# Performance work log

Measured on AMD Instinct MI355X. Metric: run time of the kernel, lower is better.

## Reference

```python
import jax, jax.numpy as jnp
import numpy as np

NEG_BIG = -9e15

def setup_inputs() -> dict:
    key = jax.random.key(0)
    k1, k2, k3, k4 = jax.random.split(key, 4)
    N, F_in, F_out = 8192, 512, 128
    return {
        "input": jax.random.normal(k1, (N, F_in), dtype=jnp.float32),
        "adj": jax.random.randint(k2, (N, N), 0, 2, dtype=jnp.int32),
        "W": jax.random.normal(k3, (F_in, F_out), dtype=jnp.float32) * 0.05,
        "a": jax.random.normal(k4, (2 * F_out, 1), dtype=jnp.float32) * 0.05,
    }

def reference(input, adj, W, a):
    alpha = 0.2  # LeakyReLU negative slope
    h = input @ W                      # [N, F_out]
    F_out = h.shape[1]
    # concat score decomposition: a^T [h_i || h_j] = h_i @ a1 + h_j @ a2
    a1 = a[:F_out, 0]                  # [F_out]
    a2 = a[F_out:, 0]                  # [F_out]
    e = jax.nn.leaky_relu(h @ a1[:, None] + (h @ a2)[None, :], negative_slope=alpha)  # [N, N]
    e = jnp.where(adj > 0, e, NEG_BIG)
    attention = jax.nn.softmax(e, axis=1)
    h_prime = attention @ h            # [N, F_out]
    return jax.nn.elu(h_prime)         # concat=True
```

## Files before the change

kernel.cpp:

```cpp
#include <hip/hip_runtime.h>
#include <hip/hip_bf16.h>


typedef __attribute__((ext_vector_type(4))) float f32x4;
typedef __attribute__((ext_vector_type(8))) short s16x8;

#define N_NODES 8192
#define F_IN 512
#define F_OUT 128
#define JS 16
#define WCOLS (N_NODES / JS)

static __device__ __forceinline__ short f2bf(float f) {
  __hip_bfloat16 h = __float2bfloat16(f);
  return __builtin_bit_cast(short, h);
}

__global__ __launch_bounds__(256) void kA(const float* __restrict__ W,
    const float* __restrict__ a, unsigned short* __restrict__ WT,
    float* __restrict__ wa) {
  int b = blockIdx.x;
  if (b < 256) {
    int idx = b * 256 + threadIdx.x;
    int k = idx >> 7, f = idx & 127;
    WT[(size_t)f * F_IN + k] = (unsigned short)f2bf(W[idx]);
  } else {
    int k = (b - 256) * 256 + threadIdx.x;
    if (k < F_IN) {
      const float* Wr = W + (size_t)k * F_OUT;
      float d1 = 0.f, d2 = 0.f;
#pragma unroll 8
      for (int f = 0; f < F_OUT; f += 4) {
        f32x4 w  = *(const f32x4*)(Wr + f);
        f32x4 a1 = *(const f32x4*)(a + f);
        f32x4 a2 = *(const f32x4*)(a + F_OUT + f);
        d1 += w[0] * a1[0] + w[1] * a1[1] + w[2] * a1[2] + w[3] * a1[3];
        d2 += w[0] * a2[0] + w[1] * a2[1] + w[2] * a2[2] + w[3] * a2[3];
      }
      wa[k] = d1;
      wa[F_IN + k] = d2;
    }
  }
}

__global__ __launch_bounds__(256) void kB(const int* __restrict__ adj,
    unsigned long long* __restrict__ mask, const float* __restrict__ X,
    const float* __restrict__ wa, const unsigned short* __restrict__ WT,
    f32x4* __restrict__ rowdat, unsigned* __restrict__ pE,
    unsigned short* __restrict__ hT) {
  int b = blockIdx.x;
  int wave = threadIdx.x >> 6, lane = threadIdx.x & 63;

  if (b < 4096) {
    const int nwaves = 4096 * 4;
    int wid = b * 4 + wave;
    const int ntasks = N_NODES * (N_NODES / 256);
    for (int task = wid; task < ntasks; task += nwaves) {
      int row = task >> 5;
      int cg = task & 31;
      const int* p = adj + (size_t)row * N_NODES + cg * 256 + lane;
      int v0 = p[0], v1 = p[64], v2 = p[128], v3 = p[192];
      unsigned long long b0 = __ballot(v0 != 0);
      unsigned long long b1 = __ballot(v1 != 0);
      unsigned long long b2 = __ballot(v2 != 0);
      unsigned long long b3 = __ballot(v3 != 0);
      if (lane == 0) {
        unsigned long long* q = mask + (size_t)row * (N_NODES / 64) + cg * 4;
        ulonglong2 w0; w0.x = b0; w0.y = b1;
        ulonglong2 w1; w1.x = b2; w1.y = b3;
        *(ulonglong2*)(q) = w0;
        *(ulonglong2*)(q + 2) = w1;
      }
    }
  } else if (b < 6144) {
    int i = (b - 4096) * 4 + wave;
    const float* Xr = X + (size_t)i * F_IN + lane * 8;
    f32x4 x0 = ((const f32x4*)Xr)[0];
    f32x4 x1 = ((const f32x4*)Xr)[1];
    f32x4 w10 = ((const f32x4*)(wa + lane * 8))[0];
    f32x4 w11 = ((const f32x4*)(wa + lane * 8))[1];
    f32x4 w20 = ((const f32x4*)(wa + F_IN + lane * 8))[0];
    f32x4 w21 = ((const f32x4*)(wa + F_IN + lane * 8))[1];
    float d1 = 0.f, d2 = 0.f;
#pragma unroll
    for (int e = 0; e < 4; e++) {
      d1 += x0[e] * w10[e] + x1[e] * w11[e];
      d2 += x0[e] * w20[e] + x1[e] * w21[e];
    }
#pragma unroll
    for (int m = 1; m < 64; m <<= 1) {
      d1 += __shfl_xor(d1, m, 64);
      d2 += __shfl_xor(d2, m, 64);
    }
    if (lane == 0) {
      float s1 = d1, s2 = d2;
      f32x4 rd;
      rd[0] = expf(s1);
      rd[1] = expf(0.2f * s1);
      rd[2] = expf(-s1);
      rd[3] = 0.f;
      rowdat[i] = rd;
      unsigned e2  = (unsigned)(unsigned short)f2bf(expf(s2));
      unsigned e2s = (unsigned)(unsigned short)f2bf(expf(0.2f * s2));
      pE[i] = (e2s << 16) | e2;
    }
  } else {
    int lrow = lane & 15, grp = lane >> 4;
    int tile = (b - 6144) * 4 + wave;
    int fb = tile & 7;
    int nb = tile >> 3;
    const unsigned short* Ar = WT + (size_t)(fb * 16 + lrow) * F_IN + grp * 8;
    const float* Br = X + (size_t)(nb * 16 + lrow) * F_IN + grp * 8;

    f32x4 acc = (f32x4)(0.0f);
#pragma unroll
    for (int k0 = 0; k0 < F_IN; k0 += 32) {
      s16x8 af = *(const s16x8*)(Ar + k0);
      f32x4 b0 = *(const f32x4*)(Br + k0);
      f32x4 b1 = *(const f32x4*)(Br + k0 + 4);
      s16x8 bf;
#pragma unroll
      for (int e = 0; e < 4; e++) { bf[e] = f2bf(b0[e]); bf[e + 4] = f2bf(b1[e]); }
      acc = __builtin_amdgcn_mfma_f32_16x16x32_bf16(af, bf, acc, 0, 0, 0);
    }
#pragma unroll
    for (int r = 0; r < 4; r++)
      hT[(size_t)(fb * 16 + grp * 4 + r) * N_NODES + nb * 16 + lrow] =
          (unsigned short)f2bf(acc[r]);
  }
}

__global__ __launch_bounds__(256, 2) void kC(const unsigned* __restrict__ mask32,
    const unsigned short* __restrict__ hT, const f32x4* __restrict__ rowdat,
    const unsigned* __restrict__ pE, float* __restrict__ accws,
    float* __restrict__ denws) {
  __shared__ float red[4][16 * 132];
  __shared__ float sden[4][4][16];

  int wave = threadIdx.x >> 6, lane = threadIdx.x & 63;
  int lrow = lane & 15, grp = lane >> 4;
  int rb = blockIdx.x >> 2;
  int q = blockIdx.x & 3;
  int js = q * 4 + wave;
  int rbase = rb * 64;
  int jlo = js * WCOLS;

  float E1[4], E1s[4], T1[4];
#pragma unroll
  for (int rt = 0; rt < 4; rt++) {
    f32x4 rd = rowdat[rbase + rt * 16 + lrow];
    E1[rt] = rd[0]; E1s[rt] = rd[1]; T1[rt] = rd[2];
  }

  f32x4 acc[4][8];
#pragma unroll
  for (int rt = 0; rt < 4; rt++)
#pragma unroll
    for (int n = 0; n < 8; n++) acc[rt][n] = (f32x4)(0.0f);
  float dsum[4] = {0.f, 0.f, 0.f, 0.f};

#define PROC1(rt, pe, e)                                              \
  {                                                                   \
    unsigned pu = (pe);                                               \
    float E2  = __builtin_bit_cast(float, pu << 16);                  \
    float E2s = __builtin_bit_cast(float, pu & 0xffff0000u);          \
    float sel = (E2 > T1[rt]) ? E1[rt] * E2 : E1s[rt] * E2s;          \
    float p = ((bm >> (e)) & 1u) ? sel : 0.f;                         \
    dsum[rt] += p;                                                    \
    af[rt][e] = f2bf(p);                                              \
  }

  for (int sc = 0; sc < 4; sc++) {
    int jb = jlo + sc * 128;
    uint4 mm[4];
#pragma unroll
    for (int rt = 0; rt < 4; rt++)
      mm[rt] = *(const uint4*)(mask32 +
          (size_t)(rbase + rt * 16 + lrow) * (N_NODES / 32) + jb / 32);

#pragma unroll
    for (int t = 0; t < 4; t++) {
      int jj = jb + t * 32 + grp * 8;
      const uint4* pp = (const uint4*)(pE + jj);
      uint4 P0 = pp[0], P1 = pp[1];
      s16x8 af[4];
#pragma unroll
      for (int rt = 0; rt < 4; rt++) {
        unsigned bm = (mm[rt][t] >> (grp * 8)) & 0xffu;
        PROC1(rt, P0.x, 0); PROC1(rt, P0.y, 1);
        PROC1(rt, P0.z, 2); PROC1(rt, P0.w, 3);
        PROC1(rt, P1.x, 4); PROC1(rt, P1.y, 5);
        PROC1(rt, P1.z, 6); PROC1(rt, P1.w, 7);
      }
#pragma unroll
      for (int n = 0; n < 8; n++) {
        s16x8 bf = *(const s16x8*)(hT + (size_t)(n * 16 + lrow) * N_NODES + jj);
#pragma unroll
        for (int rt = 0; rt < 4; rt++)
          acc[rt][n] =
              __builtin_amdgcn_mfma_f32_16x16x32_bf16(af[rt], bf, acc[rt][n], 0, 0, 0);
      }
    }
  }
#undef PROC1

#pragma unroll
  for (int rt = 0; rt < 4; rt++) {
    float d = dsum[rt];
    d += __shfl_xor(d, 16, 64);
    d += __shfl_xor(d, 32, 64);
    if (lane < 16) sden[wave][rt][lane] = d;
  }

#pragma unroll
  for (int rt = 0; rt < 4; rt++) {
    __syncthreads();
#pragma unroll
    for (int n = 0; n < 8; n++)
#pragma unroll
      for (int r = 0; r < 4; r++)
        red[wave][(grp * 4 + r) * 132 + n * 16 + lrow] = acc[rt][n][r];
    __syncthreads();
    int e0 = threadIdx.x * 8;
    int row16 = e0 >> 7, col = e0 & 127;
    int li = row16 * 132 + col;
    f32x4 s0 = *(f32x4*)&red[0][li] + *(f32x4*)&red[1][li] +
               *(f32x4*)&red[2][li] + *(f32x4*)&red[3][li];
    f32x4 s1 = *(f32x4*)&red[0][li + 4] + *(f32x4*)&red[1][li + 4] +
               *(f32x4*)&red[2][li + 4] + *(f32x4*)&red[3][li + 4];
    float* dst = accws +
        ((size_t)q * N_NODES + rbase + rt * 16 + row16) * F_OUT + col;
    *(f32x4*)dst = s0;
    *(f32x4*)(dst + 4) = s1;
  }
  __syncthreads();
  if (threadIdx.x < 64) {
    int rt = threadIdx.x >> 4, r16 = threadIdx.x & 15;
    float d = sden[0][rt][r16] + sden[1][rt][r16] +
              sden[2][rt][r16] + sden[3][rt][r16];
    denws[q * N_NODES + rbase + threadIdx.x] = d;
  }
}

__global__ void kD(const float* __restrict__ accws,
                   const float* __restrict__ denws, float* __restrict__ out) {
  int idx4 = blockIdx.x * 256 + threadIdx.x;
  int i = idx4 >> 5;
  const int S4 = N_NODES * F_OUT / 4;
  f32x4 s = (f32x4)(0.0f);
  float d = 0.f;
#pragma unroll
  for (int q = 0; q < 4; q++) {
    s += ((const f32x4*)accws)[idx4 + (size_t)q * S4];
    d += denws[i + q * N_NODES];
  }
  f32x4 v = s / d;
#pragma unroll
  for (int e = 0; e < 4; e++) v[e] = v[e] > 0.f ? v[e] : expm1f(v[e]);
  ((f32x4*)out)[idx4] = v;
}

extern "C" void kernel_launch(void* const* d_in, const int* in_sizes, int n_in,
                              void* d_out, int out_size, void* d_ws, size_t ws_size,
                              hipStream_t stream) {
  const float* X   = (const float*)d_in[0];
  const int*   adj = (const int*)d_in[1];
  const float* W   = (const float*)d_in[2];
  const float* a   = (const float*)d_in[3];
  float* out = (float*)d_out;

  char* ws = (char*)d_ws;
  size_t off = 0;
  unsigned short* WT = (unsigned short*)(ws + off); off += (size_t)F_OUT * F_IN * 2;
  unsigned short* hT = (unsigned short*)(ws + off); off += (size_t)F_OUT * N_NODES * 2;
  f32x4* rowdat = (f32x4*)(ws + off); off += (size_t)N_NODES * 16;
  unsigned* pE = (unsigned*)(ws + off); off += (size_t)N_NODES * 4;
  float* wa = (float*)(ws + off); off += (size_t)2 * F_IN * 4;
  unsigned long long* mask = (unsigned long long*)(ws + off);
  off += (size_t)N_NODES * (N_NODES / 64) * 8;
  float* accws = (float*)(ws + off); off += (size_t)4 * N_NODES * F_OUT * 4;
  float* denws = (float*)(ws + off); off += (size_t)4 * N_NODES * 4;
  (void)in_sizes; (void)n_in; (void)out_size; (void)ws_size;

  kA<<<258, 256, 0, stream>>>(W, a, WT, wa);
  kB<<<7168, 256, 0, stream>>>(adj, mask, X, wa, WT, rowdat, pE, hT);
  kC<<<(N_NODES / 64) * 4, 256, 0, stream>>>((const unsigned*)mask, hT,
                                             rowdat, pE, accws, denws);
  kD<<<(N_NODES * F_OUT) / 4 / 256, 256, 0, stream>>>(accws, denws, out);
}
```

Before: 518.7 us.

## Pre-swizzle h into MFMA fragment layout and retile attention kernel

Moves the adjacency bitmask packing into its own kernel and has the staging GEMM write h in a blob layout matching the MFMA B-fragment, so each lane loads its 16 bytes contiguously. The attention kernel is retiled: each wave handles 16 rows by 64 features across half the columns, with 2 column splits instead of 4. This removes the LDS cross-wave reduction and halves the partial-sum workspace. The cost is that the softmax weights (mask, exp, select) are now recomputed by two feature-group waves per row tile, and the mask kernel is serialized ahead of the GEMM.

```diff
diff --git a/kernel.cpp b/kernel.cpp
--- a/kernel.cpp
+++ b/kernel.cpp
@@ -8,12 +8,35 @@
 #define N_NODES 8192
 #define F_IN 512
 #define F_OUT 128
-#define JS 16
-#define WCOLS (N_NODES / JS)
 
 static __device__ __forceinline__ short f2bf(float f) {
   __hip_bfloat16 h = __float2bfloat16(f);
   return __builtin_bit_cast(short, h);
+}
+
+__global__ __launch_bounds__(256) void kMask(const int* __restrict__ adj,
+    unsigned long long* __restrict__ mask) {
+  const int nwaves = gridDim.x * 4;
+  int wid = blockIdx.x * 4 + (threadIdx.x >> 6);
+  int lane = threadIdx.x & 63;
+  const int ntasks = N_NODES * (N_NODES / 256);
+  for (int task = wid; task < ntasks; task += nwaves) {
+    int row = task >> 5;
+    int cg = task & 31;
+    const int* p = adj + (size_t)row * N_NODES + cg * 256 + lane;
+    int v0 = p[0], v1 = p[64], v2 = p[128], v3 = p[192];
+    unsigned long long b0 = __ballot(v0 != 0);
+    unsigned long long b1 = __ballot(v1 != 0);
+    unsigned long long b2 = __ballot(v2 != 0);
+    unsigned long long b3 = __ballot(v3 != 0);
+    if (lane == 0) {
+      unsigned long long* q = mask + (size_t)row * (N_NODES / 64) + cg * 4;
+      ulonglong2 w0; w0.x = b0; w0.y = b1;
+      ulonglong2 w1; w1.x = b2; w1.y = b3;
+      *(ulonglong2*)(q) = w0;
+      *(ulonglong2*)(q + 2) = w1;
+    }
+  }
 }
 
 __global__ __launch_bounds__(256) void kA(const float* __restrict__ W,
@@ -43,37 +66,39 @@
   }
 }
 
-__global__ __launch_bounds__(256) void kB(const int* __restrict__ adj,
-    unsigned long long* __restrict__ mask, const float* __restrict__ X,
+__global__ __launch_bounds__(256) void kStage(const float* __restrict__ X,
     const float* __restrict__ wa, const unsigned short* __restrict__ WT,
     f32x4* __restrict__ rowdat, unsigned* __restrict__ pE,
-    unsigned short* __restrict__ hT) {
+    unsigned short* __restrict__ blob) {
   int b = blockIdx.x;
   int wave = threadIdx.x >> 6, lane = threadIdx.x & 63;
 
-  if (b < 4096) {
-    const int nwaves = 4096 * 4;
-    int wid = b * 4 + wave;
-    const int ntasks = N_NODES * (N_NODES / 256);
-    for (int task = wid; task < ntasks; task += nwaves) {
-      int row = task >> 5;
-      int cg = task & 31;
-      const int* p = adj + (size_t)row * N_NODES + cg * 256 + lane;
-      int v0 = p[0], v1 = p[64], v2 = p[128], v3 = p[192];
-      unsigned long long b0 = __ballot(v0 != 0);
-      unsigned long long b1 = __ballot(v1 != 0);
-      unsigned long long b2 = __ballot(v2 != 0);
-      unsigned long long b3 = __ballot(v3 != 0);
-      if (lane == 0) {
-        unsigned long long* q = mask + (size_t)row * (N_NODES / 64) + cg * 4;
-        ulonglong2 w0; w0.x = b0; w0.y = b1;
-        ulonglong2 w1; w1.x = b2; w1.y = b3;
-        *(ulonglong2*)(q) = w0;
-        *(ulonglong2*)(q + 2) = w1;
-      }
-    }
-  } else if (b < 6144) {
-    int i = (b - 4096) * 4 + wave;
+  if (b < 1024) {
+    int lrow = lane & 15, grp = lane >> 4;
+    int tile = b * 4 + wave;
+    int fb = tile & 7;
+    int nb = tile >> 3;
+    const unsigned short* Ar = WT + (size_t)(fb * 16 + lrow) * F_IN + grp * 8;
+    const float* Br = X + (size_t)(nb * 16 + lrow) * F_IN + grp * 8;
+
+    f32x4 acc = (f32x4)(0.0f);
+#pragma unroll
+    for (int k0 = 0; k0 < F_IN; k0 += 32) {
+      s16x8 af = *(const s16x8*)(Ar + k0);
+      f32x4 b0 = *(const f32x4*)(Br + k0);
+      f32x4 b1 = *(const f32x4*)(Br + k0 + 4);
+      s16x8 bf;
+#pragma unroll
+      for (int e = 0; e < 4; e++) { bf[e] = f2bf(b0[e]); bf[e + 4] = f2bf(b1[e]); }
+      acc = __builtin_amdgcn_mfma_f32_16x16x32_bf16(af, bf, acc, 0, 0, 0);
+    }
+    int cc = (nb & 1) * 16 + lrow;
+    size_t bl = ((size_t)(fb * 256 + (nb >> 1)) * 64 + (cc >> 3) * 16 + grp * 4);
+#pragma unroll
+    for (int r = 0; r < 4; r++)
+      blob[(bl + r) * 8 + (lrow & 7)] = (unsigned short)f2bf(acc[r]);
+  } else {
+    int i = (b - 1024) * 4 + wave;
     const float* Xr = X + (size_t)i * F_IN + lane * 8;
     f32x4 x0 = ((const f32x4*)Xr)[0];
     f32x4 x1 = ((const f32x4*)Xr)[1];
@@ -104,142 +129,77 @@
       unsigned e2s = (unsigned)(unsigned short)f2bf(expf(0.2f * s2));
       pE[i] = (e2s << 16) | e2;
     }
-  } else {
-    int lrow = lane & 15, grp = lane >> 4;
-    int tile = (b - 6144) * 4 + wave;
-    int fb = tile & 7;
-    int nb = tile >> 3;
-    const unsigned short* Ar = WT + (size_t)(fb * 16 + lrow) * F_IN + grp * 8;
-    const float* Br = X + (size_t)(nb * 16 + lrow) * F_IN + grp * 8;
-
-    f32x4 acc = (f32x4)(0.0f);
-#pragma unroll
-    for (int k0 = 0; k0 < F_IN; k0 += 32) {
-      s16x8 af = *(const s16x8*)(Ar + k0);
-      f32x4 b0 = *(const f32x4*)(Br + k0);
-      f32x4 b1 = *(const f32x4*)(Br + k0 + 4);
-      s16x8 bf;
-#pragma unroll
-      for (int e = 0; e < 4; e++) { bf[e] = f2bf(b0[e]); bf[e + 4] = f2bf(b1[e]); }
-      acc = __builtin_amdgcn_mfma_f32_16x16x32_bf16(af, bf, acc, 0, 0, 0);
-    }
-#pragma unroll
-    for (int r = 0; r < 4; r++)
-      hT[(size_t)(fb * 16 + grp * 4 + r) * N_NODES + nb * 16 + lrow] =
-          (unsigned short)f2bf(acc[r]);
-  }
-}
-
-__global__ __launch_bounds__(256, 2) void kC(const unsigned* __restrict__ mask32,
-    const unsigned short* __restrict__ hT, const f32x4* __restrict__ rowdat,
-    const unsigned* __restrict__ pE, float* __restrict__ accws,
-    float* __restrict__ denws) {
-  __shared__ float red[4][16 * 132];
-  __shared__ float sden[4][4][16];
-
+  }
+}
+
+__global__ __launch_bounds__(256, 2) void kCompute(
+    const unsigned* __restrict__ mask32, const unsigned short* __restrict__ blob,
+    const f32x4* __restrict__ rowdat, const unsigned* __restrict__ pE,
+    float* __restrict__ accws, float* __restrict__ denws) {
   int wave = threadIdx.x >> 6, lane = threadIdx.x & 63;
   int lrow = lane & 15, grp = lane >> 4;
-  int rb = blockIdx.x >> 2;
-  int q = blockIdx.x & 3;
-  int js = q * 4 + wave;
-  int rbase = rb * 64;
-  int jlo = js * WCOLS;
-
-  float E1[4], E1s[4], T1[4];
-#pragma unroll
-  for (int rt = 0; rt < 4; rt++) {
-    f32x4 rd = rowdat[rbase + rt * 16 + lrow];
-    E1[rt] = rd[0]; E1s[rt] = rd[1]; T1[rt] = rd[2];
-  }
-
-  f32x4 acc[4][8];
-#pragma unroll
-  for (int rt = 0; rt < 4; rt++)
-#pragma unroll
-    for (int n = 0; n < 8; n++) acc[rt][n] = (f32x4)(0.0f);
-  float dsum[4] = {0.f, 0.f, 0.f, 0.f};
-
-#define PROC1(rt, pe, e)                                              \
-  {                                                                   \
-    unsigned pu = (pe);                                               \
-    float E2  = __builtin_bit_cast(float, pu << 16);                  \
-    float E2s = __builtin_bit_cast(float, pu & 0xffff0000u);          \
-    float sel = (E2 > T1[rt]) ? E1[rt] * E2 : E1s[rt] * E2s;          \
-    float p = ((bm >> (e)) & 1u) ? sel : 0.f;                         \
-    dsum[rt] += p;                                                    \
-    af[rt][e] = f2bf(p);                                              \
-  }
-
-  for (int sc = 0; sc < 4; sc++) {
-    int jb = jlo + sc * 128;
+  int rb = blockIdx.x >> 1;
+  int js = blockIdx.x & 1;
+  int rowtile = wave & 1, fg = wave >> 1;
+  int row = rb * 32 + rowtile * 16 + lrow;
+
+  f32x4 rd = rowdat[row];
+  float E1 = rd[0], E1s = rd[1], T1 = rd[2];
+
+  f32x4 acc[4];
+#pragma unroll
+  for (int nt = 0; nt < 4; nt++) acc[nt] = (f32x4)(0.0f);
+  float dsum = 0.f;
+
+  const unsigned* mrow = mask32 + (size_t)row * (N_NODES / 32) + js * 128;
+
+  for (int o = 0; o < 8; o++) {
     uint4 mm[4];
-#pragma unroll
-    for (int rt = 0; rt < 4; rt++)
-      mm[rt] = *(const uint4*)(mask32 +
-          (size_t)(rbase + rt * 16 + lrow) * (N_NODES / 32) + jb / 32);
-
-#pragma unroll
-    for (int t = 0; t < 4; t++) {
-      int jj = jb + t * 32 + grp * 8;
-      const uint4* pp = (const uint4*)(pE + jj);
-      uint4 P0 = pp[0], P1 = pp[1];
-      s16x8 af[4];
-#pragma unroll
-      for (int rt = 0; rt < 4; rt++) {
-        unsigned bm = (mm[rt][t] >> (grp * 8)) & 0xffu;
-        PROC1(rt, P0.x, 0); PROC1(rt, P0.y, 1);
-        PROC1(rt, P0.z, 2); PROC1(rt, P0.w, 3);
-        PROC1(rt, P1.x, 4); PROC1(rt, P1.y, 5);
-        PROC1(rt, P1.z, 6); PROC1(rt, P1.w, 7);
+    const uint4* mp = (const uint4*)(mrow + o * 16);
+#pragma unroll
+    for (int q = 0; q < 4; q++) mm[q] = mp[q];
+
+#pragma unroll
+    for (int c = 0; c < 16; c++) {
+      int ct = js * 128 + o * 16 + c;
+      int j0 = ct * 32 + grp * 8;
+      unsigned w = mm[c >> 2][c & 3];
+      uint4 P0 = *(const uint4*)(pE + j0);
+      uint4 P1 = *(const uint4*)(pE + j0 + 4);
+      s16x8 af;
+#define PROCE(pw, e)                                                  \
+      {                                                               \
+        unsigned pu = (pw);                                           \
+        float E2  = __builtin_bit_cast(float, pu << 16);              \
+        float E2s = __builtin_bit_cast(float, pu & 0xffff0000u);      \
+        float sel = (E2 > T1) ? E1 * E2 : E1s * E2s;                  \
+        float p = ((w >> (grp * 8 + (e))) & 1u) ? sel : 0.f;          \
+        dsum += p;                                                    \
+        af[e] = f2bf(p);                                              \
       }
-#pragma unroll
-      for (int n = 0; n < 8; n++) {
-        s16x8 bf = *(const s16x8*)(hT + (size_t)(n * 16 + lrow) * N_NODES + jj);
-#pragma unroll
-        for (int rt = 0; rt < 4; rt++)
-          acc[rt][n] =
-              __builtin_amdgcn_mfma_f32_16x16x32_bf16(af[rt], bf, acc[rt][n], 0, 0, 0);
+      PROCE(P0.x, 0) PROCE(P0.y, 1) PROCE(P0.z, 2) PROCE(P0.w, 3)
+      PROCE(P1.x, 4) PROCE(P1.y, 5) PROCE(P1.z, 6) PROCE(P1.w, 7)
+#undef PROCE
+#pragma unroll
+      for (int nt = 0; nt < 4; nt++) {
+        s16x8 bf = *(const s16x8*)(blob +
+            (((size_t)(fg * 4 + nt) * 256 + ct) * 64 + lane) * 8);
+        acc[nt] = __builtin_amdgcn_mfma_f32_16x16x32_bf16(af, bf, acc[nt], 0, 0, 0);
       }
     }
   }
-#undef PROC1
-
-#pragma unroll
-  for (int rt = 0; rt < 4; rt++) {
-    float d = dsum[rt];
-    d += __shfl_xor(d, 16, 64);
-    d += __shfl_xor(d, 32, 64);
-    if (lane < 16) sden[wave][rt][lane] = d;
-  }
-
-#pragma unroll
-  for (int rt = 0; rt < 4; rt++) {
-    __syncthreads();
-#pragma unroll
-    for (int n = 0; n < 8; n++)
-#pragma unroll
-      for (int r = 0; r < 4; r++)
-        red[wave][(grp * 4 + r) * 132 + n * 16 + lrow] = acc[rt][n][r];
-    __syncthreads();
-    int e0 = threadIdx.x * 8;
-    int row16 = e0 >> 7, col = e0 & 127;
-    int li = row16 * 132 + col;
-    f32x4 s0 = *(f32x4*)&red[0][li] + *(f32x4*)&red[1][li] +
-               *(f32x4*)&red[2][li] + *(f32x4*)&red[3][li];
-    f32x4 s1 = *(f32x4*)&red[0][li + 4] + *(f32x4*)&red[1][li + 4] +
-               *(f32x4*)&red[2][li + 4] + *(f32x4*)&red[3][li + 4];
-    float* dst = accws +
-        ((size_t)q * N_NODES + rbase + rt * 16 + row16) * F_OUT + col;
-    *(f32x4*)dst = s0;
-    *(f32x4*)(dst + 4) = s1;
-  }
-  __syncthreads();
-  if (threadIdx.x < 64) {
-    int rt = threadIdx.x >> 4, r16 = threadIdx.x & 15;
-    float d = sden[0][rt][r16] + sden[1][rt][r16] +
-              sden[2][rt][r16] + sden[3][rt][r16];
-    denws[q * N_NODES + rbase + threadIdx.x] = d;
-  }
+
+  dsum += __shfl_xor(dsum, 16, 64);
+  dsum += __shfl_xor(dsum, 32, 64);
+  if (fg == 0 && lane < 16)
+    denws[js * N_NODES + rb * 32 + rowtile * 16 + lane] = dsum;
+
+#pragma unroll
+  for (int nt = 0; nt < 4; nt++)
+#pragma unroll
+    for (int r = 0; r < 4; r++)
+      accws[((size_t)js * N_NODES + rb * 32 + rowtile * 16 + grp * 4 + r) * F_OUT +
+            fg * 64 + nt * 16 + lrow] = acc[nt][r];
 }
 
 __global__ void kD(const float* __restrict__ accws,
@@ -247,13 +207,8 @@
   int idx4 = blockIdx.x * 256 + threadIdx.x;
   int i = idx4 >> 5;
   const int S4 = N_NODES * F_OUT / 4;
-  f32x4 s = (f32x4)(0.0f);
-  float d = 0.f;
-#pragma unroll
-  for (int q = 0; q < 4; q++) {
-    s += ((const f32x4*)accws)[idx4 + (size_t)q * S4];
-    d += denws[i + q * N_NODES];
-  }
+  f32x4 s = ((const f32x4*)accws)[idx4] + ((const f32x4*)accws)[idx4 + S4];
+  float d = denws[i] + denws[i + N_NODES];
   f32x4 v = s / d;
 #pragma unroll
   for (int e = 0; e < 4; e++) v[e] = v[e] > 0.f ? v[e] : expm1f(v[e]);
@@ -272,19 +227,20 @@
   char* ws = (char*)d_ws;
   size_t off = 0;
   unsigned short* WT = (unsigned short*)(ws + off); off += (size_t)F_OUT * F_IN * 2;
-  unsigned short* hT = (unsigned short*)(ws + off); off += (size_t)F_OUT * N_NODES * 2;
+  unsigned short* blob = (unsigned short*)(ws + off); off += (size_t)F_OUT * N_NODES * 2;
   f32x4* rowdat = (f32x4*)(ws + off); off += (size_t)N_NODES * 16;
   unsigned* pE = (unsigned*)(ws + off); off += (size_t)N_NODES * 4;
   float* wa = (float*)(ws + off); off += (size_t)2 * F_IN * 4;
   unsigned long long* mask = (unsigned long long*)(ws + off);
   off += (size_t)N_NODES * (N_NODES / 64) * 8;
-  float* accws = (float*)(ws + off); off += (size_t)4 * N_NODES * F_OUT * 4;
-  float* denws = (float*)(ws + off); off += (size_t)4 * N_NODES * 4;
+  float* accws = (float*)(ws + off); off += (size_t)2 * N_NODES * F_OUT * 4;
+  float* denws = (float*)(ws + off); off += (size_t)2 * N_NODES * 4;
   (void)in_sizes; (void)n_in; (void)out_size; (void)ws_size;
 
+  kMask<<<2048, 256, 0, stream>>>(adj, mask);
   kA<<<258, 256, 0, stream>>>(W, a, WT, wa);
-  kB<<<7168, 256, 0, stream>>>(adj, mask, X, wa, WT, rowdat, pE, hT);
-  kC<<<(N_NODES / 64) * 4, 256, 0, stream>>>((const unsigned*)mask, hT,
-                                             rowdat, pE, accws, denws);
+  kStage<<<3072, 256, 0, stream>>>(X, wa, WT, rowdat, pE, blob);
+  kCompute<<<(N_NODES / 32) * 2, 256, 0, stream>>>((const unsigned*)mask, blob,
+                                                   rowdat, pE, accws, denws);
   kD<<<(N_NODES * F_OUT) / 4 / 256, 256, 0, stream>>>(accws, denws, out);
 }
```

After: 581.2 us. 12.1% more time.
